# Kernel optimization log

Hardware: AMD Instinct MI355X
Metric: run time of the kernel (lower is better)

The kernel has to match this reference:

```python
import jax, jax.numpy as jnp
import numpy as np

N = 8192
IN_C = 256
OUT_C = 64
ALPHA = 0.2  # LeakyReLU negative slope
NEG_INF = -9e15


def setup_inputs() -> dict:
    key = jax.random.key(0)
    k1, k2, k3, k4 = jax.random.split(key, 4)
    x = jax.random.normal(k1, (N, IN_C), dtype=jnp.float32)
    adjacent = jax.random.randint(k2, (N, N), 0, 2, dtype=jnp.int32)
    # xavier_uniform with gain=1.2: limit = gain * sqrt(6/(fan_in+fan_out))
    lim_w = 1.2 * np.sqrt(6.0 / (IN_C + OUT_C))
    w = jax.random.uniform(k3, (IN_C, OUT_C), dtype=jnp.float32, minval=-lim_w, maxval=lim_w)
    lim_a = 1.2 * np.sqrt(6.0 / (2 * OUT_C + 1))
    a = jax.random.uniform(k4, (2 * OUT_C, 1), dtype=jnp.float32, minval=-lim_a, maxval=lim_a)
    return {"x": x, "adjacent": adjacent, "w": w, "a": a}


def reference(x, adjacent, w, a):
    # h: [N, out]
    h = x @ w
    # e_ij = LeakyReLU(a^T [h_i || h_j]) computed without materializing [N,N,2*out]:
    # split a into source/target halves -> rank-1 broadcast sum.
    a_src = a[:OUT_C, 0]   # [out]
    a_dst = a[OUT_C:, 0]   # [out]
    f_src = h @ a_src      # [N]
    f_dst = h @ a_dst      # [N]
    e = f_src[:, None] + f_dst[None, :]            # [N, N]
    e = jnp.where(e > 0, e, ALPHA * e)             # LeakyReLU
    # mask by adjacency, softmax over neighbors (rows)
    e = jnp.where(adjacent > 0, e, NEG_INF)
    attention = jax.nn.softmax(e, axis=-1)         # [N, N]
    h_prime = attention @ h                        # [N, out]
    # concat=True -> ELU activation
    return jax.nn.elu(h_prime)
```

## Files before the change

### kernel.cpp

```cpp
#include <hip/hip_runtime.h>
#include <hip/hip_bf16.h>

#define N 8192
#define IN_C 256
#define OUT_C 64
#define ALPHA 0.2f
#define L2E 1.44269504f

typedef short bf16x8 __attribute__((ext_vector_type(8)));
typedef float f32x4 __attribute__((ext_vector_type(4)));
typedef unsigned long long u64;

#define OFF_H      0u
#define OFF_HT     2097152u
#define OFF_FS     3145728u
#define OFF_FD     3178496u
#define OFF_FDMAX  3211264u
#define OFF_BITS   3211520u
#define OFF_NUM    11600128u

__global__ __launch_bounds__(256) void k_linear(const float* __restrict__ x,
                                                const float* __restrict__ w,
                                                const float* __restrict__ a,
                                                float* __restrict__ h,
                                                float* __restrict__ fs,
                                                float* __restrict__ fd) {
    __shared__ float wl[IN_C * OUT_C];
    int t = threadIdx.x;
    for (int idx = t; idx < IN_C * OUT_C; idx += 256) wl[idx] = w[idx];
    __syncthreads();
    int i = blockIdx.x * 4 + (t >> 6);
    int c = t & 63;
    const float* xr = x + (size_t)i * IN_C;
    float acc = 0.f;
#pragma unroll 8
    for (int k = 0; k < IN_C; ++k) acc = fmaf(xr[k], wl[k * 64 + c], acc);
    h[(size_t)i * 64 + c] = acc;
    float s = acc * a[c];
    float d = acc * a[64 + c];
#pragma unroll
    for (int off = 32; off > 0; off >>= 1) {
        s += __shfl_xor(s, off, 64);
        d += __shfl_xor(d, off, 64);
    }
    if (c == 0) { fs[i] = s; fd[i] = d; }
}

__global__ __launch_bounds__(256) void k_frag(const float* __restrict__ h,
                                              unsigned short* __restrict__ htf) {
    __shared__ float lds[64 * 65];
    int t = threadIdx.x;
    int i0 = blockIdx.x * 64;
#pragma unroll
    for (int k = 0; k < 16; ++k) {
        int idx = k * 256 + t;
        int il = idx >> 6, c = idx & 63;
        lds[c * 65 + il] = h[(size_t)(i0 + il) * 64 + c];
    }
    __syncthreads();
    int l = t & 63;
    int ct = t >> 6;
    int r = l & 15, kg = l >> 4;
    int ch = ct * 16 + r;
#pragma unroll
    for (int ksl = 0; ksl < 2; ++ksl) {
        int ks = blockIdx.x * 2 + ksl;
        int n0 = ksl * 32 + kg * 8;
        bf16x8 v;
#pragma unroll
        for (int e = 0; e < 8; ++e) {
            __hip_bfloat16 hb = __float2bfloat16(lds[ch * 65 + n0 + e]);
            union { __hip_bfloat16 b; short s16; } u; u.b = hb;
            v[e] = u.s16;
        }
        *(bf16x8*)(htf + ((size_t)(ks * 4 + ct) * 64 + l) * 8) = v;
    }
}

__global__ __launch_bounds__(256) void k_fdmax(const float* __restrict__ fd,
                                               float* __restrict__ out) {
    __shared__ float red[256];
    int t = threadIdx.x;
    float m = -3.4e38f;
    for (int j = t; j < N; j += 256) m = fmaxf(m, fd[j]);
    red[t] = m;
    __syncthreads();
    for (int s = 128; s > 0; s >>= 1) {
        if (t < s) red[t] = fmaxf(red[t], red[t + s]);
        __syncthreads();
    }
    if (t == 0) out[0] = red[0];
}

__global__ __launch_bounds__(256) void k_pack(const int* __restrict__ adj,
                                              u64* __restrict__ bits) {
    const int NW = 2048 * 4;
    int t = threadIdx.x;
    int l = t & 63;
    int wv = (blockIdx.x * 256 + t) >> 6;
#pragma unroll 1
    for (int c = wv; c < (N / 256) * N / 1; c += 2 * NW) {
        int4 v0 = *(const int4*)(adj + (size_t)c * 256 + l * 4);
        int4 v1 = *(const int4*)(adj + (size_t)(c + NW) * 256 + l * 4);
        u64 a0 = __ballot(v0.x > 0), a1 = __ballot(v0.y > 0);
        u64 a2 = __ballot(v0.z > 0), a3 = __ballot(v0.w > 0);
        u64 b0 = __ballot(v1.x > 0), b1 = __ballot(v1.y > 0);
        u64 b2 = __ballot(v1.z > 0), b3 = __ballot(v1.w > 0);
        if (l == 0) {
            u64* q0 = bits + (size_t)c * 4;
            q0[0] = a0; q0[1] = a1; q0[2] = a2; q0[3] = a3;
            u64* q1 = bits + (size_t)(c + NW) * 4;
            q1[0] = b0; q1[1] = b1; q1[2] = b2; q1[3] = b3;
        }
    }
}

struct HStage {
    float4 fd0, fd1;
    bf16x8 b0, b1, b2, b3;
};

__device__ __forceinline__ void load_h2(HStage& s,
        const float* __restrict__ fdst,
        const unsigned short* __restrict__ hb,
        int jb, int ksg) {
    s.fd0 = *(const float4*)(fdst + jb);
    s.fd1 = *(const float4*)(fdst + jb + 4);
    const unsigned short* p = hb + (size_t)ksg * 2048;
    s.b0 = *(const bf16x8*)(p);
    s.b1 = *(const bf16x8*)(p + 512);
    s.b2 = *(const bf16x8*)(p + 1024);
    s.b3 = *(const bf16x8*)(p + 1536);
}

__device__ __forceinline__ void compute_h(const HStage& s,
        u64 m0, u64 m1, u64 m2, u64 m3, int k8, int kg2,
        float fs, float mL, const bf16x8& bones,
        f32x4& acc0, f32x4& acc1, f32x4& acc2, f32x4& acc3, f32x4& acc4) {
    float fdv[8] = {s.fd0.x, s.fd0.y, s.fd0.z, s.fd0.w, s.fd1.x, s.fd1.y, s.fd1.z, s.fd1.w};
    u64 msel[4] = {m0, m1, m2, m3};
    bf16x8 af;
#pragma unroll
    for (int e = 0; e < 8; ++e) {
        int sh = k8 * 8 + kg2 + (e >> 2);
        unsigned bit = (unsigned)(msel[e & 3] >> sh) & 1u;
        float ee = fs + fdv[e];
        float l  = fmaxf(ee, ALPHA * ee);
        float a2 = __builtin_fmaf(l, L2E, -mL);
        float wt = __builtin_amdgcn_exp2f(a2);
        wt = bit ? wt : 0.f;
        __hip_bfloat16 hb = __float2bfloat16(wt);
        union { __hip_bfloat16 b; short s16; } u; u.b = hb;
        af[e] = u.s16;
    }
    acc0 = __builtin_amdgcn_mfma_f32_16x16x32_bf16(af, s.b0, acc0, 0, 0, 0);
    acc1 = __builtin_amdgcn_mfma_f32_16x16x32_bf16(af, s.b1, acc1, 0, 0, 0);
    acc2 = __builtin_amdgcn_mfma_f32_16x16x32_bf16(af, s.b2, acc2, 0, 0, 0);
    acc3 = __builtin_amdgcn_mfma_f32_16x16x32_bf16(af, s.b3, acc3, 0, 0, 0);
    acc4 = __builtin_amdgcn_mfma_f32_16x16x32_bf16(af, bones, acc4, 0, 0, 0);
}

__global__ __launch_bounds__(256, 4) void k_mfma(
    const u64* __restrict__ bitsg,
    const float* __restrict__ fsrc,
    const float* __restrict__ fdst,
    const float* __restrict__ fdmax_p,
    const unsigned short* __restrict__ htf,
    float* __restrict__ nump,
    float* __restrict__ denp_out,
    int jch, int ns, int groups) {
    __shared__ u64 bits[64 * 34];
    int bid = blockIdx.x;
    int rb = bid & 127, kq = bid >> 7;
    int t = threadIdx.x, w = t >> 6, l = t & 63;
    int r = l & 15, kg = l >> 4, kg2 = kg * 2;
    int ib0 = rb * 64;
    int i = ib0 + w * 16 + r;
    int j0 = kq * jch;
    int strideU = groups * 4 + 2;
    int gw = groups * 4;
    int gbase4 = (j0 >> 8) * 4;

    for (int u = t; u < 64 * gw; u += 256) {
        int rowL = u / gw, rem = u - rowL * gw;
        bits[rowL * strideU + rem] = bitsg[(size_t)(ib0 + rowL) * 128 + gbase4 + rem];
    }
    __syncthreads();

    float fs  = fsrc[i];
    float fdm = *fdmax_p;
    float e0  = fs + fdm;
    float m   = fmaxf(e0, ALPHA * e0);
    float mL  = m * L2E;

    const unsigned short* hb = htf + l * 8;
    int ks0 = j0 >> 5;

    bf16x8 bones;
#pragma unroll
    for (int e = 0; e < 8; ++e) bones[e] = (short)0x3F80;

    f32x4 acc0 = {0.f,0.f,0.f,0.f}, acc1 = {0.f,0.f,0.f,0.f};
    f32x4 acc2 = {0.f,0.f,0.f,0.f}, acc3 = {0.f,0.f,0.f,0.f};
    f32x4 acc4 = {0.f,0.f,0.f,0.f};

    int baseJ = j0 + kg * 8;
    int rowL = w * 16 + r;
    HStage A, B;
    load_h2(A, fdst, hb, baseJ, ks0);
    load_h2(B, fdst, hb, baseJ + 32, ks0 + 1);

#pragma unroll 1
    for (int g = 0; g < groups; ++g) {
        const u64* mp = &bits[rowL * strideU + g * 4];
        u64 m0 = mp[0], m1 = mp[1], m2 = mp[2], m3 = mp[3];
#pragma unroll
        for (int k8 = 0; k8 < 8; ++k8) {
            int ks = g * 8 + k8;
            int nxt = ks + 2 < ns ? ks + 2 : 0;
            if (k8 & 1) {
                compute_h(B, m0, m1, m2, m3, k8, kg2, fs, mL, bones,
                          acc0, acc1, acc2, acc3, acc4);
                load_h2(B, fdst, hb, baseJ + nxt * 32, ks0 + nxt);
            } else {
                compute_h(A, m0, m1, m2, m3, k8, kg2, fs, mL, bones,
                          acc0, acc1, acc2, acc3, acc4);
                load_h2(A, fdst, hb, baseJ + nxt * 32, ks0 + nxt);
            }
        }
    }

    int orow = ib0 + w * 16 + kg * 4;
    float* np = nump + (size_t)kq * N * 64;
#pragma unroll
    for (int rr = 0; rr < 4; ++rr) {
        np[(size_t)(orow + rr) * 64 + 0 * 16 + r] = acc0[rr];
        np[(size_t)(orow + rr) * 64 + 1 * 16 + r] = acc1[rr];
        np[(size_t)(orow + rr) * 64 + 2 * 16 + r] = acc2[rr];
        np[(size_t)(orow + rr) * 64 + 3 * 16 + r] = acc3[rr];
    }
    if (r == 0) {
#pragma unroll
        for (int rr = 0; rr < 4; ++rr) denp_out[kq * N + orow + rr] = acc4[rr];
    }
}

__global__ __launch_bounds__(256) void k_final(const float* __restrict__ nump,
                                               const float* __restrict__ denp,
                                               float* __restrict__ out,
                                               int kqn) {
    int gid = blockIdx.x * 256 + threadIdx.x;
    int base = gid * 4;
    int i = base >> 6;
    float4 num = {0.f, 0.f, 0.f, 0.f};
    float den = 0.f;
    for (int q = 0; q < kqn; ++q) {
        float4 v = *(const float4*)(nump + (size_t)q * (N * 64) + base);
        num.x += v.x; num.y += v.y; num.z += v.z; num.w += v.w;
        den += denp[q * N + i];
    }
    float rd = 1.f / den;
    float4 o;
    o.x = num.x * rd; o.y = num.y * rd; o.z = num.z * rd; o.w = num.w * rd;
    o.x = o.x > 0.f ? o.x : __expf(o.x) - 1.f;
    o.y = o.y > 0.f ? o.y : __expf(o.y) - 1.f;
    o.z = o.z > 0.f ? o.z : __expf(o.z) - 1.f;
    o.w = o.w > 0.f ? o.w : __expf(o.w) - 1.f;
    *(float4*)(out + base) = o;
}

extern "C" void kernel_launch(void* const* d_in, const int* in_sizes, int n_in,
                              void* d_out, int out_size, void* d_ws, size_t ws_size,
                              hipStream_t stream) {
    const float* x   = (const float*)d_in[0];
    const int*   adj = (const int*)d_in[1];
    const float* w   = (const float*)d_in[2];
    const float* a   = (const float*)d_in[3];
    float* out = (float*)d_out;
    char*  ws  = (char*)d_ws;

    float*          h    = (float*)(ws + OFF_H);
    unsigned short* htf  = (unsigned short*)(ws + OFF_HT);
    float*          fs   = (float*)(ws + OFF_FS);
    float*          fd   = (float*)(ws + OFF_FD);
    float*          fdm  = (float*)(ws + OFF_FDMAX);
    u64*            bits = (u64*)(ws + OFF_BITS);
    float*          nump = (float*)(ws + OFF_NUM);

    size_t need8 = (size_t)OFF_NUM + 8ull * N * 64 * 4 + 8ull * N * 4;
    int KQ = (ws_size >= need8) ? 8 : 4;
    float* denp = nump + (size_t)KQ * N * 64;
    int jch = N / KQ;
    int ns  = jch / 32;
    int groups = jch / 256;

    k_linear<<<2048, 256, 0, stream>>>(x, w, a, h, fs, fd);
    k_frag<<<128, 256, 0, stream>>>(h, htf);
    k_fdmax<<<1, 256, 0, stream>>>(fd, fdm);
    k_pack<<<2048, 256, 0, stream>>>(adj, bits);
    k_mfma<<<KQ * 128, 256, 0, stream>>>(bits, fs, fd, fdm, htf, nump, denp,
                                         jch, ns, groups);
    k_final<<<512, 256, 0, stream>>>(nump, denp, out, KQ);
}
```

Baseline: 511.8 us.

## Stage h tiles through LDS with async global_load_lds ring buffer

Result: faster. 500.4 us (-2.2%).

```diff
diff --git a/kernel.cpp b/kernel.cpp
--- a/kernel.cpp
+++ b/kernel.cpp
@@ -94,70 +94,37 @@
 
 __global__ __launch_bounds__(256) void k_pack(const int* __restrict__ adj,
                                               u64* __restrict__ bits) {
-    const int NW = 2048 * 4;
-    int t = threadIdx.x;
-    int l = t & 63;
+    int t = threadIdx.x, l = t & 63;
     int wv = (blockIdx.x * 256 + t) >> 6;
+    const int NWV = 2048 * 4;
 #pragma unroll 1
-    for (int c = wv; c < (N / 256) * N / 1; c += 2 * NW) {
-        int4 v0 = *(const int4*)(adj + (size_t)c * 256 + l * 4);
-        int4 v1 = *(const int4*)(adj + (size_t)(c + NW) * 256 + l * 4);
-        u64 a0 = __ballot(v0.x > 0), a1 = __ballot(v0.y > 0);
-        u64 a2 = __ballot(v0.z > 0), a3 = __ballot(v0.w > 0);
-        u64 b0 = __ballot(v1.x > 0), b1 = __ballot(v1.y > 0);
-        u64 b2 = __ballot(v1.z > 0), b3 = __ballot(v1.w > 0);
+    for (int base = wv * 4; base < 262144; base += NWV * 4) {
+        int4 v0 = *(const int4*)(adj + (size_t)(base + 0) * 256 + l * 4);
+        int4 v1 = *(const int4*)(adj + (size_t)(base + 1) * 256 + l * 4);
+        int4 v2 = *(const int4*)(adj + (size_t)(base + 2) * 256 + l * 4);
+        int4 v3 = *(const int4*)(adj + (size_t)(base + 3) * 256 + l * 4);
+        u64 b00 = __ballot(v0.x > 0), b01 = __ballot(v0.y > 0);
+        u64 b02 = __ballot(v0.z > 0), b03 = __ballot(v0.w > 0);
+        u64 b10 = __ballot(v1.x > 0), b11 = __ballot(v1.y > 0);
+        u64 b12 = __ballot(v1.z > 0), b13 = __ballot(v1.w > 0);
+        u64 b20 = __ballot(v2.x > 0), b21 = __ballot(v2.y > 0);
+        u64 b22 = __ballot(v2.z > 0), b23 = __ballot(v2.w > 0);
+        u64 b30 = __ballot(v3.x > 0), b31 = __ballot(v3.y > 0);
+        u64 b32 = __ballot(v3.z > 0), b33 = __ballot(v3.w > 0);
         if (l == 0) {
-            u64* q0 = bits + (size_t)c * 4;
-            q0[0] = a0; q0[1] = a1; q0[2] = a2; q0[3] = a3;
-            u64* q1 = bits + (size_t)(c + NW) * 4;
-            q1[0] = b0; q1[1] = b1; q1[2] = b2; q1[3] = b3;
+            u64* q = bits + (size_t)base * 4;
+            q[0] = b00; q[1] = b01; q[2]  = b02; q[3]  = b03;
+            q[4] = b10; q[5] = b11; q[6]  = b12; q[7]  = b13;
+            q[8] = b20; q[9] = b21; q[10] = b22; q[11] = b23;
+            q[12] = b30; q[13] = b31; q[14] = b32; q[15] = b33;
         }
     }
 }
 
-struct HStage {
-    float4 fd0, fd1;
-    bf16x8 b0, b1, b2, b3;
-};
-
-__device__ __forceinline__ void load_h2(HStage& s,
-        const float* __restrict__ fdst,
-        const unsigned short* __restrict__ hb,
-        int jb, int ksg) {
-    s.fd0 = *(const float4*)(fdst + jb);
-    s.fd1 = *(const float4*)(fdst + jb + 4);
-    const unsigned short* p = hb + (size_t)ksg * 2048;
-    s.b0 = *(const bf16x8*)(p);
-    s.b1 = *(const bf16x8*)(p + 512);
-    s.b2 = *(const bf16x8*)(p + 1024);
-    s.b3 = *(const bf16x8*)(p + 1536);
-}
-
-__device__ __forceinline__ void compute_h(const HStage& s,
-        u64 m0, u64 m1, u64 m2, u64 m3, int k8, int kg2,
-        float fs, float mL, const bf16x8& bones,
-        f32x4& acc0, f32x4& acc1, f32x4& acc2, f32x4& acc3, f32x4& acc4) {
-    float fdv[8] = {s.fd0.x, s.fd0.y, s.fd0.z, s.fd0.w, s.fd1.x, s.fd1.y, s.fd1.z, s.fd1.w};
-    u64 msel[4] = {m0, m1, m2, m3};
-    bf16x8 af;
-#pragma unroll
-    for (int e = 0; e < 8; ++e) {
-        int sh = k8 * 8 + kg2 + (e >> 2);
-        unsigned bit = (unsigned)(msel[e & 3] >> sh) & 1u;
-        float ee = fs + fdv[e];
-        float l  = fmaxf(ee, ALPHA * ee);
-        float a2 = __builtin_fmaf(l, L2E, -mL);
-        float wt = __builtin_amdgcn_exp2f(a2);
-        wt = bit ? wt : 0.f;
-        __hip_bfloat16 hb = __float2bfloat16(wt);
-        union { __hip_bfloat16 b; short s16; } u; u.b = hb;
-        af[e] = u.s16;
-    }
-    acc0 = __builtin_amdgcn_mfma_f32_16x16x32_bf16(af, s.b0, acc0, 0, 0, 0);
-    acc1 = __builtin_amdgcn_mfma_f32_16x16x32_bf16(af, s.b1, acc1, 0, 0, 0);
-    acc2 = __builtin_amdgcn_mfma_f32_16x16x32_bf16(af, s.b2, acc2, 0, 0, 0);
-    acc3 = __builtin_amdgcn_mfma_f32_16x16x32_bf16(af, s.b3, acc3, 0, 0, 0);
-    acc4 = __builtin_amdgcn_mfma_f32_16x16x32_bf16(af, bones, acc4, 0, 0, 0);
+__device__ __forceinline__ void stage16(const unsigned short* g, unsigned short* lds) {
+    __builtin_amdgcn_global_load_lds(
+        (const __attribute__((address_space(1))) unsigned int*)g,
+        (__attribute__((address_space(3))) unsigned int*)lds, 16, 0, 0);
 }
 
 __global__ __launch_bounds__(256, 4) void k_mfma(
@@ -170,6 +137,8 @@
     float* __restrict__ denp_out,
     int jch, int ns, int groups) {
     __shared__ u64 bits[64 * 34];
+    __shared__ float fd_lds[1024];
+    __shared__ alignas(16) unsigned short bufs[4][2048];
     int bid = blockIdx.x;
     int rb = bid & 127, kq = bid >> 7;
     int t = threadIdx.x, w = t >> 6, l = t & 63;
@@ -180,11 +149,13 @@
     int strideU = groups * 4 + 2;
     int gw = groups * 4;
     int gbase4 = (j0 >> 8) * 4;
+    bool fdl = (jch <= 1024);
 
     for (int u = t; u < 64 * gw; u += 256) {
         int rowL = u / gw, rem = u - rowL * gw;
         bits[rowL * strideU + rem] = bitsg[(size_t)(ib0 + rowL) * 128 + gbase4 + rem];
     }
+    if (fdl) for (int u = t; u < jch; u += 256) fd_lds[u] = fdst[j0 + u];
     __syncthreads();
 
     float fs  = fsrc[i];
@@ -193,8 +164,10 @@
     float m   = fmaxf(e0, ALPHA * e0);
     float mL  = m * L2E;
 
-    const unsigned short* hb = htf + l * 8;
     int ks0 = j0 >> 5;
+    stage16(htf + ((size_t)(ks0 + 0) * 2048 + t * 8), &bufs[0][w * 512]);
+    stage16(htf + ((size_t)(ks0 + 1) * 2048 + t * 8), &bufs[1][w * 512]);
+    stage16(htf + ((size_t)(ks0 + 2) * 2048 + t * 8), &bufs[2][w * 512]);
 
     bf16x8 bones;
 #pragma unroll
@@ -204,29 +177,56 @@
     f32x4 acc2 = {0.f,0.f,0.f,0.f}, acc3 = {0.f,0.f,0.f,0.f};
     f32x4 acc4 = {0.f,0.f,0.f,0.f};
 
-    int baseJ = j0 + kg * 8;
     int rowL = w * 16 + r;
-    HStage A, B;
-    load_h2(A, fdst, hb, baseJ, ks0);
-    load_h2(B, fdst, hb, baseJ + 32, ks0 + 1);
-
 #pragma unroll 1
     for (int g = 0; g < groups; ++g) {
         const u64* mp = &bits[rowL * strideU + g * 4];
         u64 m0 = mp[0], m1 = mp[1], m2 = mp[2], m3 = mp[3];
+        u64 msel[4] = {m0, m1, m2, m3};
 #pragma unroll
         for (int k8 = 0; k8 < 8; ++k8) {
             int ks = g * 8 + k8;
-            int nxt = ks + 2 < ns ? ks + 2 : 0;
-            if (k8 & 1) {
-                compute_h(B, m0, m1, m2, m3, k8, kg2, fs, mL, bones,
-                          acc0, acc1, acc2, acc3, acc4);
-                load_h2(B, fdst, hb, baseJ + nxt * 32, ks0 + nxt);
+            if (ks < ns - 2)       asm volatile("s_waitcnt vmcnt(2)" ::: "memory");
+            else if (ks == ns - 2) asm volatile("s_waitcnt vmcnt(1)" ::: "memory");
+            else                   asm volatile("s_waitcnt vmcnt(0)" ::: "memory");
+            asm volatile("s_barrier" ::: "memory");
+            if (ks + 3 < ns)
+                stage16(htf + ((size_t)(ks0 + ks + 3) * 2048 + t * 8),
+                        &bufs[(ks + 3) & 3][w * 512]);
+
+            const unsigned short* bp = &bufs[ks & 3][0];
+            bf16x8 b0 = *(const bf16x8*)(bp + (0 * 64 + l) * 8);
+            bf16x8 b1 = *(const bf16x8*)(bp + (1 * 64 + l) * 8);
+            bf16x8 b2 = *(const bf16x8*)(bp + (2 * 64 + l) * 8);
+            bf16x8 b3 = *(const bf16x8*)(bp + (3 * 64 + l) * 8);
+            float4 fd0, fd1;
+            if (fdl) {
+                fd0 = *(const float4*)(fd_lds + ks * 32 + kg * 8);
+                fd1 = *(const float4*)(fd_lds + ks * 32 + kg * 8 + 4);
             } else {
-                compute_h(A, m0, m1, m2, m3, k8, kg2, fs, mL, bones,
-                          acc0, acc1, acc2, acc3, acc4);
-                load_h2(A, fdst, hb, baseJ + nxt * 32, ks0 + nxt);
+                fd0 = *(const float4*)(fdst + j0 + ks * 32 + kg * 8);
+                fd1 = *(const float4*)(fdst + j0 + ks * 32 + kg * 8 + 4);
             }
+            float fdv[8] = {fd0.x, fd0.y, fd0.z, fd0.w, fd1.x, fd1.y, fd1.z, fd1.w};
+            bf16x8 af;
+#pragma unroll
+            for (int e = 0; e < 8; ++e) {
+                int sh = k8 * 8 + kg2 + (e >> 2);
+                unsigned bit = (unsigned)(msel[e & 3] >> sh) & 1u;
+                float ee = fs + fdv[e];
+                float lv = fmaxf(ee, ALPHA * ee);
+                float a2 = __builtin_fmaf(lv, L2E, -mL);
+                float wt = __builtin_amdgcn_exp2f(a2);
+                wt = bit ? wt : 0.f;
+                __hip_bfloat16 hb = __float2bfloat16(wt);
+                union { __hip_bfloat16 b; short s16; } u; u.b = hb;
+                af[e] = u.s16;
+            }
+            acc0 = __builtin_amdgcn_mfma_f32_16x16x32_bf16(af, b0, acc0, 0, 0, 0);
+            acc1 = __builtin_amdgcn_mfma_f32_16x16x32_bf16(af, b1, acc1, 0, 0, 0);
+            acc2 = __builtin_amdgcn_mfma_f32_16x16x32_bf16(af, b2, acc2, 0, 0, 0);
+            acc3 = __builtin_amdgcn_mfma_f32_16x16x32_bf16(af, b3, acc3, 0, 0, 0);
+            acc4 = __builtin_amdgcn_mfma_f32_16x16x32_bf16(af, bones, acc4, 0, 0, 0);
         }
     }
 
```
